# Kernel tuning notes

Measured on AMD Instinct MI355X. Metric: run time of the kernel, lower is better.

The kernel has to match this reference:

```python
import jax, jax.numpy as jnp
import numpy as np
import math

N = 8192
F_IN = 1024
F_OUT = 1024
MAX_ITER = 10


def whale_optimizer(positions, key, max_iter=MAX_ITER):
    """Vectorized whale optimization algorithm.

    Faithful to the original per-agent/per-dim update rules, but the agent
    loop is vectorized (on-device RNG, one parallel update per outer
    iteration); only the `max_iter` outer iterations stay sequential.
    positions: [N, D] float32.
    """
    n, d = positions.shape
    lower = jnp.min(positions)
    upper = jnp.max(positions)
    k0, loop_key = jax.random.split(key)
    leader = positions[jax.random.randint(k0, (), 0, n)]  # [D]

    def step(carry, it):
        pos, leader = carry
        itf = it.astype(jnp.float32)
        k = jax.random.fold_in(loop_key, it)
        k1, k2, k3, k4, k5, k6 = jax.random.split(k, 6)
        a = 2.0 - itf * (2.0 / max_iter)
        a2 = -1.0 + itf * (-1.0 / max_iter)
        r1 = jax.random.uniform(k1, (n, 1))
        r2 = jax.random.uniform(k2, (n, 1))
        A = 2.0 * a * r1 - a                       # [n,1]
        C = 2.0 * r2                               # [n,1]
        lp = (a2 - 1.0) * jax.random.uniform(k3, (n, 1)) + 1.0  # spiral param
        p = jax.random.uniform(k4, (n, 1))
        # random leader per (agent, dim), as in the original inner j-loop
        ridx = jax.random.randint(k5, (n, d), 0, n)
        x_rand = jnp.take_along_axis(pos, ridx, axis=0)         # [n,d]
        explore = jnp.abs(x_rand - A * jnp.abs(C * x_rand - pos))
        exploit = jnp.abs(leader - A * jnp.abs(C * leader - pos))
        spiral = jnp.abs(jnp.abs(leader - pos) * jnp.exp(lp) * jnp.cos(2.0 * jnp.pi * lp) + leader)
        new_pos = jnp.where(p < 0.5,
                            jnp.where(jnp.abs(A) >= 1.0, explore, exploit),
                            spiral)
        new_pos = jnp.clip(new_pos, lower, upper)
        new_leader = new_pos[jax.random.randint(k6, (), 0, n)]
        return (new_pos, new_leader), None

    (positions, _), _ = jax.lax.scan(step, (positions, leader), jnp.arange(max_iter))
    return positions


def setup_inputs() -> dict:
    key = jax.random.key(0)
    k1, k2, k3, k4 = jax.random.split(key, 4)
    stdv = 1.0 / math.sqrt(F_OUT)
    return {
        "input": jax.random.normal(k1, (N, F_IN), dtype=jnp.float32),
        "adj": jax.random.uniform(k2, (N, N), dtype=jnp.float32) * (1.0 / N),
        "h0": jax.random.normal(k3, (N, F_IN), dtype=jnp.float32),
        "weight": jax.random.uniform(k4, (F_IN, F_OUT), dtype=jnp.float32,
                                      minval=-stdv, maxval=stdv),
        "lamda": jnp.float32(0.5),
        "alpha": jnp.float32(0.1),
        "l": 1,
    }


def reference(input, adj, h0, weight, lamda, alpha, l):
    # variant=False, residual=False
    theta = jnp.log(lamda / l + 1.0)
    hi = adj @ input                                  # spmm(adj, input)
    support = (1.0 - alpha) * hi + alpha * h0
    r = support
    # original detaches support before the whale optimizer
    opt = whale_optimizer(jax.lax.stop_gradient(support), jax.random.key(42))
    output = theta * (opt @ weight) + (1.0 - theta) * r
    return output
```

## Files before the change

kernel.cpp:

```cpp
#include <hip/hip_runtime.h>
#include <hip/hip_bf16.h>
#include <stdint.h>
#include <math.h>

typedef uint32_t u32;
typedef __hip_bfloat16 bf16t;
typedef __attribute__((ext_vector_type(8))) short short8;
typedef __attribute__((ext_vector_type(4))) float f32x4;


__host__ __device__ __forceinline__ void tf2(u32 k0, u32 k1, u32 c0, u32 c1, u32& o0, u32& o1) {
  const u32 ks2 = k0 ^ k1 ^ 0x1BD11BDAu;
  u32 x0 = c0 + k0, x1 = c1 + k1;
#define TFROT(v,r) (((v)<<(r))|((v)>>(32-(r))))
#define TFR(r) { x0 += x1; x1 = TFROT(x1,r); x1 ^= x0; }
  TFR(13) TFR(15) TFR(26) TFR(6)   x0 += k1;  x1 += ks2 + 1u;
  TFR(17) TFR(29) TFR(16) TFR(24)  x0 += ks2; x1 += k0 + 2u;
  TFR(13) TFR(15) TFR(26) TFR(6)   x0 += k0;  x1 += k1 + 3u;
  TFR(17) TFR(29) TFR(16) TFR(24)  x0 += k1;  x1 += ks2 + 4u;
  TFR(13) TFR(15) TFR(26) TFR(6)   x0 += ks2; x1 += k0 + 5u;
#undef TFR
#undef TFROT
  o0 = x0; o1 = x1;
}

__host__ __device__ __forceinline__ float unif_row(u32 ka, u32 kb, int i) {
  u32 o0, o1;
  tf2(ka, kb, 0u, (u32)i, o0, o1);
  return __uint_as_float(0x3F800000u | ((o0 ^ o1) >> 9)) - 1.0f;
}

__device__ __forceinline__ int ridx_fn(u32 ka, u32 kb, u32 f) {
  u32 o0, o1; tf2(ka, kb, 0u, f, o0, o1); return (int)((o0 ^ o1) & 8191u);
}

static inline void split2(u32 ka, u32 kb, u32* kA, u32* kB) {
  u32 a0, a1, b0, b1;
  tf2(ka, kb, 0u, 0u, a0, a1);
  tf2(ka, kb, 0u, 1u, b0, b1);
  kA[0] = a0; kA[1] = a1; kB[0] = b0; kB[1] = b1;
}

static inline void split6(u32 ka, u32 kb, u32 out[6][2]) {
  for (u32 i = 0; i < 6; i++) { u32 o0, o1; tf2(ka, kb, 0u, i, o0, o1); out[i][0] = o0; out[i][1] = o1; }
}

static inline int scalar_randint8192(u32 ka, u32 kb) {
  u32 kA[2], kB[2];
  split2(ka, kb, kA, kB);
  u32 o0, o1;
  tf2(kB[0], kB[1], 0u, 0u, o0, o1);
  return (int)((o0 ^ o1) & 8191u);
}

__host__ __device__ __forceinline__ ushort f2bf(float f) {
  u32 u = __float_as_uint(f);
  u32 r = u + 0x7FFFu + ((u >> 16) & 1u);
  return (ushort)(r >> 16);
}

__device__ __forceinline__ void packa_body(int idx, const float* __restrict__ A, uint4* __restrict__ out,
                                           int K, int lgS) {
  const int S = K >> 6;
  const int chunk = idx >> 10;
  const int w = idx & 1023;
  const int r = w >> 3, kq = w & 7;
  const int cm = chunk >> lgS, s = chunk & (S - 1);
  const float* src = A + (size_t)((cm << 7) + r) * K + (s << 6) + (kq << 3);
  const float4 f0 = *(const float4*)src;
  const float4 f1 = *(const float4*)(src + 4);
  u32 wv[4];
  wv[0] = (u32)f2bf(f0.x) | ((u32)f2bf(f0.y) << 16);
  wv[1] = (u32)f2bf(f0.z) | ((u32)f2bf(f0.w) << 16);
  wv[2] = (u32)f2bf(f1.x) | ((u32)f2bf(f1.y) << 16);
  wv[3] = (u32)f2bf(f1.z) | ((u32)f2bf(f1.w) << 16);
  uint4 o; o.x = wv[0]; o.y = wv[1]; o.z = wv[2]; o.w = wv[3];
  out[((size_t)chunk << 10) + (r << 3) + (kq ^ (r & 7))] = o;
}

__device__ __forceinline__ void packb_body(int idx, const float* __restrict__ B, uint4* __restrict__ out,
                                           int Nn) {
  const int g = idx / Nn;
  const int n = idx - g * Nn;
  u32 wv[4];
#pragma unroll
  for (int j = 0; j < 4; j++) {
    const float f0 = B[(size_t)(g * 8 + 2 * j) * Nn + n];
    const float f1 = B[(size_t)(g * 8 + 2 * j + 1) * Nn + n];
    wv[j] = (u32)f2bf(f0) | ((u32)f2bf(f1) << 16);
  }
  uint4 o; o.x = wv[0]; o.y = wv[1]; o.z = wv[2]; o.w = wv[3];
  out[idx] = o;
}

__global__ __launch_bounds__(256) void pack_all_k(
    const float* __restrict__ adj, uint4* __restrict__ apk,
    const float* __restrict__ inp, uint4* __restrict__ b1p,
    const float* __restrict__ wgt, uint4* __restrict__ wp) {
  const int b = blockIdx.x;
  const int tid = threadIdx.x;
  if (b < 32768) {
    packa_body(b * 256 + tid, adj, apk, 8192, 7);
  } else if (b < 36864) {
    packb_body((b - 32768) * 256 + tid, inp, b1p, 1024);
  } else {
    packb_body((b - 36864) * 256 + tid, wgt, wp, 1024);
  }
}

__global__ __launch_bounds__(256) void minmax2_k(const float* __restrict__ part, int G, float* __restrict__ bnd) {
  __shared__ float slo[256], shi[256];
  const int tid = threadIdx.x;
  float lo = 3.4e38f, hi = -3.4e38f;
  for (int i = tid; i < G; i += 256) { lo = fminf(lo, part[i]); hi = fmaxf(hi, part[G + i]); }
  slo[tid] = lo; shi[tid] = hi; __syncthreads();
  for (int s = 128; s > 0; s >>= 1) {
    if (tid < s) { slo[tid] = fminf(slo[tid], slo[tid + s]); shi[tid] = fmaxf(shi[tid], shi[tid + s]); }
    __syncthreads();
  }
  if (tid == 0) { bnd[0] = slo[0]; bnd[1] = shi[0]; }
}

__device__ __forceinline__ void gld_lds16(const void* g, void* l) {
  __builtin_amdgcn_global_load_lds((const __attribute__((address_space(1))) void*)g,
                                   (__attribute__((address_space(3))) void*)l, 16, 0, 0);
}

template <int EPI>
__global__ __launch_bounds__(256, 2) void gemm_k(
    const bf16t* __restrict__ Ap, const bf16t* __restrict__ Bp,
    const float* __restrict__ aux, const float* __restrict__ sF,
    const int* __restrict__ sI, float* __restrict__ C,
    float* __restrict__ prt, int PG, int Nn, int K) {
  __shared__ __align__(16) bf16t As[2][8192];
  __shared__ __align__(16) bf16t Bs[2][8192];
  const int tid = threadIdx.x;
  const int lane = tid & 63;
  const int wave = tid >> 6;
  const int bm = blockIdx.x & 63;
  const int bn = blockIdx.x >> 6;
  const int m0 = bm << 7, n0 = bn << 7;
  const int wm = (wave & 1) << 6;
  const int wn = (wave >> 1) << 6;
  const int S = K >> 6;

  f32x4 acc[4][4];
#pragma unroll
  for (int i = 0; i < 4; i++)
#pragma unroll
    for (int j = 0; j < 4; j++) acc[i][j] = (f32x4){0.f, 0.f, 0.f, 0.f};

  const bf16t* gA0 = Ap + (((size_t)bm * S) << 13);
  const bf16t* gBj[4];
  const size_t bstep = (size_t)Nn * 64;
#pragma unroll
  for (int j = 0; j < 4; j++) {
    const int u = tid + (j << 8);
    gBj[j] = Bp + ((size_t)(u >> 7) * Nn + n0 + (u & 127)) * 8;
  }
  auto stage = [&](int s, int buf) {
    const bf16t* a = gA0 + ((size_t)s << 13);
#pragma unroll
    for (int j = 0; j < 4; j++) {
      const int u = tid + (j << 8);
      gld_lds16(a + ((size_t)u << 3), &As[buf][u << 3]);
    }
#pragma unroll
    for (int j = 0; j < 4; j++) {
      const int u = tid + (j << 8);
      gld_lds16(gBj[j] + (size_t)s * bstep, &Bs[buf][u << 3]);
    }
  };

  const int arow = lane & 15, aq = lane >> 4;
  const int abase = ((wm + arow) << 6) + ((aq ^ (arow & 7)) << 3);
  const int bbase = ((aq << 7) + wn + arow) << 3;

  stage(0, 0);

  for (int s = 0; s < S; ++s) {
    const int cur = s & 1;
    __syncthreads();
    if (s + 1 < S) stage(s + 1, cur ^ 1);
#pragma unroll
    for (int c = 0; c < 2; ++c) {
      short8 af[4], bv[4];
      const int ab = abase ^ (c << 5);
#pragma unroll
      for (int mt = 0; mt < 4; mt++)
        af[mt] = *(const short8*)(&As[cur][ab + mt * 1024]);
#pragma unroll
      for (int nt = 0; nt < 4; nt++)
        bv[nt] = *(const short8*)(&Bs[cur][bbase + (c << 12) + (nt << 7)]);
#pragma unroll
      for (int mt = 0; mt < 4; mt++)
#pragma unroll
        for (int nt = 0; nt < 4; nt++)
          acc[mt][nt] = __builtin_amdgcn_mfma_f32_16x16x32_bf16(af[mt], bv[nt], acc[mt][nt], 0, 0, 0);
    }
  }

  float p1, p2;
  if (EPI == 1) { const float al = sF[0]; p1 = 1.0f - al; p2 = al; }
  else { const float th = logf(sF[0] / (float)sI[0] + 1.0f); p1 = th; p2 = 1.0f - th; }
  const int col = lane & 15, rq = lane >> 4;
  float vlo = 3.4e38f, vhi = -3.4e38f;
#pragma unroll
  for (int mt = 0; mt < 4; mt++)
#pragma unroll
    for (int nt = 0; nt < 4; nt++)
#pragma unroll
      for (int r = 0; r < 4; r++) {
        const int gm = m0 + wm + mt * 16 + (rq << 2) + r;
        const int gn = n0 + wn + nt * 16 + col;
        const size_t ix = (size_t)gm * Nn + gn;
        const float v = p1 * acc[mt][nt][r] + p2 * aux[ix];
        C[ix] = v;
        if (EPI == 1) { vlo = fminf(vlo, v); vhi = fmaxf(vhi, v); }
      }
  if (EPI == 1) {
    __syncthreads();
    float* red = (float*)&As[0][0];
    red[tid] = vlo; red[256 + tid] = vhi;
    __syncthreads();
    for (int s = 128; s > 0; s >>= 1) {
      if (tid < s) {
        red[tid] = fminf(red[tid], red[tid + s]);
        red[256 + tid] = fmaxf(red[256 + tid], red[256 + tid + s]);
      }
      __syncthreads();
    }
    if (tid == 0) { prt[blockIdx.x] = red[0]; prt[PG + blockIdx.x] = red[256]; }
  }
}

struct WA {
  u32 k1a, k1b, k2a, k2b, k3a, k3b, k4a, k4b, k5a, k5b;
  int ldr;
  float a, a2;
};
struct WP { u32 k1a, k1b, k2a, k2b, k3a, k3b, k4a, k4b; float a, a2; int ldr; };
struct F5 { WP w[5]; };

__global__ __launch_bounds__(256) void whale_k(
    const float* __restrict__ pinb, float* __restrict__ poutb,
    ushort* __restrict__ opt, const float* __restrict__ bnd, WA w) {
  const int tid = threadIdx.x;
  const int wave = tid >> 6, lane = tid & 63;
  const int row = (blockIdx.x << 2) + wave;
  const float lo = bnd[0], hi = bnd[1];
  const float r1 = unif_row(w.k1a, w.k1b, row);
  const float r2 = unif_row(w.k2a, w.k2b, row);
  const float u3 = unif_row(w.k3a, w.k3b, row);
  const float p  = unif_row(w.k4a, w.k4b, row);
  float t2 = (2.0f * w.a) * r1;
  asm volatile("" : "+v"(t2));
  const float A = t2 - w.a;
  const float Cc = 2.0f * r2;
  const float* pin = pinb + ((size_t)row << 10);
  float4 pv[4];
#pragma unroll
  for (int k = 0; k < 4; ++k) pv[k] = *(const float4*)(pin + ((lane + (k << 6)) << 2));

  float ov[4][4];
  const bool bp = (p < 0.5f);
  const bool ex = bp && (fabsf(A) >= 1.0f);
  if (ex) {
    int ri[4][4];
#pragma unroll
    for (int k = 0; k < 4; ++k) {
      const u32 fb = ((u32)row << 10) + (u32)((lane + (k << 6)) << 2);
#pragma unroll
      for (int e = 0; e < 4; ++e) ri[k][e] = ridx_fn(w.k5a, w.k5b, fb + (u32)e);
    }
    float xr[4][4];
#pragma unroll
    for (int k = 0; k < 4; ++k) {
      const int j0 = (lane + (k << 6)) << 2;
#pragma unroll
      for (int e = 0; e < 4; ++e) xr[k][e] = pinb[((size_t)ri[k][e] << 10) + j0 + e];
    }
#pragma unroll
    for (int k = 0; k < 4; ++k)
#pragma unroll
      for (int e = 0; e < 4; ++e) {
        const float pos = (&pv[k].x)[e];
        ov[k][e] = fabsf(xr[k][e] - A * fabsf(Cc * xr[k][e] - pos));
      }
  } else {
    const float* ldp = pinb + ((size_t)w.ldr << 10);
    float4 lv[4];
#pragma unroll
    for (int k = 0; k < 4; ++k) lv[k] = *(const float4*)(ldp + ((lane + (k << 6)) << 2));
    if (bp) {
#pragma unroll
      for (int k = 0; k < 4; ++k)
#pragma unroll
        for (int e = 0; e < 4; ++e) {
          const float pos = (&pv[k].x)[e], ld = (&lv[k].x)[e];
          ov[k][e] = fabsf(ld - A * fabsf(Cc * ld - pos));
        }
    } else {
      const float lp = (w.a2 - 1.0f) * u3 + 1.0f;
      const float s1 = expf(lp);
      const float s2 = cosf(6.2831855f * lp);
#pragma unroll
      for (int k = 0; k < 4; ++k)
#pragma unroll
        for (int e = 0; e < 4; ++e) {
          const float pos = (&pv[k].x)[e], ld = (&lv[k].x)[e];
          ov[k][e] = fabsf(fabsf(ld - pos) * s1 * s2 + ld);
        }
    }
  }
#pragma unroll
  for (int k = 0; k < 4; ++k) {
    const int j0 = (lane + (k << 6)) << 2;
    float4 res;
#pragma unroll
    for (int e = 0; e < 4; ++e) (&res.x)[e] = fminf(fmaxf(ov[k][e], lo), hi);
    if (!opt) {
      *(float4*)(poutb + ((size_t)row << 10) + j0) = res;
    } else {
      ushort4 o4;
      o4.x = f2bf(res.x); o4.y = f2bf(res.y); o4.z = f2bf(res.z); o4.w = f2bf(res.w);
      const int rw = row & 127;
      const size_t chunk = (size_t)((row >> 7) << 4) + (j0 >> 6);
      ushort* dst = opt + (chunk << 13) + (rw << 6) + ((((j0 >> 3) & 7) ^ (rw & 7)) << 3) + (j0 & 7);
      *(ushort4*)dst = o4;
    }
  }
}

template <int NK>
__device__ __forceinline__ void upd_row(const WP w, int row, float lo, float hi,
                                        const float4* lv, float4* x) {
  const float r1 = unif_row(w.k1a, w.k1b, row);
  const float r2 = unif_row(w.k2a, w.k2b, row);
  const float u3 = unif_row(w.k3a, w.k3b, row);
  const float p  = unif_row(w.k4a, w.k4b, row);
  float t2 = (2.0f * w.a) * r1;
  asm volatile("" : "+v"(t2));
  const float A = t2 - w.a;
  const float Cc = 2.0f * r2;
  const bool bp = (p < 0.5f);
  float s1 = 0.f, s2 = 0.f;
  if (!bp) {
    const float lp = (w.a2 - 1.0f) * u3 + 1.0f;
    s1 = expf(lp);
    s2 = cosf(6.2831855f * lp);
  }
#pragma unroll
  for (int k = 0; k < NK; ++k)
#pragma unroll
    for (int e = 0; e < 4; ++e) {
      const float pos = (&x[k].x)[e], ld = (&lv[k].x)[e];
      const float ov = bp ? fabsf(ld - A * fabsf(Cc * ld - pos))
                          : fabsf(fabsf(ld - pos) * s1 * s2 + ld);
      (&x[k].x)[e] = fminf(fmaxf(ov, lo), hi);
    }
}

__global__ __launch_bounds__(256) void ldrchain_k(
    const float* __restrict__ p4, const float* __restrict__ bnd,
    float* __restrict__ V, F5 f) {
  const int j0 = threadIdx.x << 2;
  const float lo = bnd[0], hi = bnd[1];
  float4 v[5];
  v[0] = *(const float4*)(p4 + ((size_t)f.w[0].ldr << 10) + j0);
  *(float4*)(V + j0) = v[0];
#pragma unroll
  for (int t = 1; t < 5; ++t) {
    const int row = f.w[t].ldr;
    float4 x = *(const float4*)(p4 + ((size_t)row << 10) + j0);
#pragma unroll
    for (int q = 0; q < t; ++q) upd_row<1>(f.w[q], row, lo, hi, &v[q], &x);
    v[t] = x;
    *(float4*)(V + (t << 10) + j0) = x;
  }
}

__global__ __launch_bounds__(256) void fused5_k(
    const float* __restrict__ p4, const float* __restrict__ V,
    const float* __restrict__ bnd, ushort* __restrict__ opt, F5 f) {
  const int tid = threadIdx.x;
  const int wave = tid >> 6, lane = tid & 63;
  const int row = (blockIdx.x << 2) + wave;
  const float lo = bnd[0], hi = bnd[1];
  const float* pin = p4 + ((size_t)row << 10);
  float4 x[4];
#pragma unroll
  for (int k = 0; k < 4; ++k) x[k] = *(const float4*)(pin + ((lane + (k << 6)) << 2));
#pragma unroll
  for (int it = 0; it < 5; ++it) {
    float4 lv[4];
#pragma unroll
    for (int k = 0; k < 4; ++k)
      lv[k] = *(const float4*)(V + (it << 10) + ((lane + (k << 6)) << 2));
    upd_row<4>(f.w[it], row, lo, hi, lv, x);
  }
#pragma unroll
  for (int k = 0; k < 4; ++k) {
    const int j0 = (lane + (k << 6)) << 2;
    ushort4 o4;
    o4.x = f2bf(x[k].x); o4.y = f2bf(x[k].y); o4.z = f2bf(x[k].z); o4.w = f2bf(x[k].w);
    const int rw = row & 127;
    const size_t chunk = (size_t)((row >> 7) << 4) + (j0 >> 6);
    ushort* dst = opt + (chunk << 13) + (rw << 6) + ((((j0 >> 3) & 7) ^ (rw & 7)) << 3) + (j0 & 7);
    *(ushort4*)dst = o4;
  }
}

extern "C" void kernel_launch(void* const* d_in, const int* in_sizes, int n_in,
                              void* d_out, int out_size, void* d_ws, size_t ws_size,
                              hipStream_t stream) {
  const float* inp = (const float*)d_in[0];
  const float* adj = (const float*)d_in[1];
  const float* h0  = (const float*)d_in[2];
  const float* wgt = (const float*)d_in[3];
  const float* lam = (const float*)d_in[4];
  const float* alp = (const float*)d_in[5];
  const int* lint  = (const int*)d_in[6];

  float* outp = (float*)d_out;

  char* ws = (char*)d_ws;
  bf16t* Apk  = (bf16t*)(ws);
  float* P0   = (float*)(ws);
  float* P1   = (float*)(ws + 33554432);
  ushort* OPT = (ushort*)(ws + 67108864);
  bf16t* B1p  = (bf16t*)(ws + 134217728);
  bf16t* Wp   = (bf16t*)(ws + 150994944);
  float* SUP  = (float*)(ws + 153092096);
  float* PRT  = (float*)(ws + 186646528);
  float* BND  = (float*)(ws + 186662912);
  float* LDRV = (float*)(ws + 186663168);

  hipLaunchKernelGGL(pack_all_k, dim3(37376), dim3(256), 0, stream,
                     adj, (uint4*)Apk, inp, (uint4*)B1p, wgt, (uint4*)Wp);
  hipLaunchKernelGGL((gemm_k<1>), dim3(512), dim3(256), 0, stream, Apk, B1p, h0, alp, lint,
                     SUP, PRT, 512, 1024, 8192);
  hipLaunchKernelGGL(minmax2_k, dim3(1), dim3(256), 0, stream, PRT, 512, BND);

  u32 k0k[2], lpk[2];
  split2(0u, 42u, k0k, lpk);
  int ldr = scalar_randint8192(k0k[0], k0k[1]);
  WA wa[10];
  for (int it = 0; it < 10; ++it) {
    u32 ka, kb; tf2(lpk[0], lpk[1], 0u, (u32)it, ka, kb);
    u32 ks[6][2];
    split6(ka, kb, ks);
    u32 k5A[2], k5B[2];
    split2(ks[4][0], ks[4][1], k5A, k5B);
    WA& w = wa[it];
    w.k1a = ks[0][0]; w.k1b = ks[0][1];
    w.k2a = ks[1][0]; w.k2b = ks[1][1];
    w.k3a = ks[2][0]; w.k3b = ks[2][1];
    w.k4a = ks[3][0]; w.k4b = ks[3][1];
    w.k5a = k5B[0];   w.k5b = k5B[1];
    w.ldr = ldr;
    const float itf = (float)it;
    w.a = 2.0f - itf * 0.2f;
    w.a2 = -1.0f + itf * (-0.1f);
    ldr = scalar_randint8192(ks[5][0], ks[5][1]);
  }
  bool safe5 = true;
  for (int r = 0; r < 8192 && safe5; ++r) {
    u32 o0, o1; tf2(wa[5].k1a, wa[5].k1b, 0u, (u32)r, o0, o1);
    if (((o0 ^ o1) >> 9) == 0u) safe5 = false;
  }

  const float* cur = SUP;
  float* bufs[2] = {P0, P1};
  for (int it = 0; it < 5; ++it) {
    float* nxt = bufs[it & 1];
    hipLaunchKernelGGL(whale_k, dim3(2048), dim3(256), 0, stream, cur, nxt,
                       (ushort*)nullptr, BND, wa[it]);
    cur = nxt;
  }
  if (safe5) {
    F5 f;
    for (int t = 0; t < 5; ++t) {
      const WA& w = wa[5 + t];
      f.w[t].k1a = w.k1a; f.w[t].k1b = w.k1b;
      f.w[t].k2a = w.k2a; f.w[t].k2b = w.k2b;
      f.w[t].k3a = w.k3a; f.w[t].k3b = w.k3b;
      f.w[t].k4a = w.k4a; f.w[t].k4b = w.k4b;
      f.w[t].a = w.a; f.w[t].a2 = w.a2; f.w[t].ldr = w.ldr;
    }
    hipLaunchKernelGGL(ldrchain_k, dim3(1), dim3(256), 0, stream, cur, BND, LDRV, f);
    hipLaunchKernelGGL(fused5_k, dim3(2048), dim3(256), 0, stream, cur, LDRV, BND, OPT, f);
  } else {
    for (int it = 5; it < 10; ++it) {
      float* nxt = bufs[it & 1];
      hipLaunchKernelGGL(whale_k, dim3(2048), dim3(256), 0, stream, cur, nxt,
                         (it == 9) ? OPT : (ushort*)nullptr, BND, wa[it]);
      cur = nxt;
    }
  }
  hipLaunchKernelGGL((gemm_k<2>), dim3(512), dim3(256), 0, stream, (const bf16t*)OPT, Wp, SUP, lam, lint,
                     outp, (float*)nullptr, 0, 1024, 1024);
  (void)in_sizes; (void)n_in; (void)out_size; (void)ws_size;
}
```

Baseline: 857.0 us.

## Fuse fp32-to-bf16 conversion of adj into the first GEMM's A-tile loading

Removes the separate pack pass that converted the 8192x8192 fp32 adjacency matrix to a swizzled bf16 layout. The first GEMM now loads fp32 A tiles straight from global memory into registers and converts them with v_cvt_pk_bf16_f32. The next tile's loads are issued before the MFMA loop and written to LDS after it, so load latency overlaps compute. This drops a 256MB read plus a 128MB write and re-read of packed data, but raises register pressure and puts the conversion and LDS stores inside the GEMM main loop.

```diff
diff --git a/kernel.cpp b/kernel.cpp
--- a/kernel.cpp
+++ b/kernel.cpp
@@ -59,25 +59,6 @@
   return (ushort)(r >> 16);
 }
 
-__device__ __forceinline__ void packa_body(int idx, const float* __restrict__ A, uint4* __restrict__ out,
-                                           int K, int lgS) {
-  const int S = K >> 6;
-  const int chunk = idx >> 10;
-  const int w = idx & 1023;
-  const int r = w >> 3, kq = w & 7;
-  const int cm = chunk >> lgS, s = chunk & (S - 1);
-  const float* src = A + (size_t)((cm << 7) + r) * K + (s << 6) + (kq << 3);
-  const float4 f0 = *(const float4*)src;
-  const float4 f1 = *(const float4*)(src + 4);
-  u32 wv[4];
-  wv[0] = (u32)f2bf(f0.x) | ((u32)f2bf(f0.y) << 16);
-  wv[1] = (u32)f2bf(f0.z) | ((u32)f2bf(f0.w) << 16);
-  wv[2] = (u32)f2bf(f1.x) | ((u32)f2bf(f1.y) << 16);
-  wv[3] = (u32)f2bf(f1.z) | ((u32)f2bf(f1.w) << 16);
-  uint4 o; o.x = wv[0]; o.y = wv[1]; o.z = wv[2]; o.w = wv[3];
-  out[((size_t)chunk << 10) + (r << 3) + (kq ^ (r & 7))] = o;
-}
-
 __device__ __forceinline__ void packb_body(int idx, const float* __restrict__ B, uint4* __restrict__ out,
                                            int Nn) {
   const int g = idx / Nn;
@@ -94,17 +75,14 @@
 }
 
 __global__ __launch_bounds__(256) void pack_all_k(
-    const float* __restrict__ adj, uint4* __restrict__ apk,
     const float* __restrict__ inp, uint4* __restrict__ b1p,
     const float* __restrict__ wgt, uint4* __restrict__ wp) {
   const int b = blockIdx.x;
   const int tid = threadIdx.x;
-  if (b < 32768) {
-    packa_body(b * 256 + tid, adj, apk, 8192, 7);
-  } else if (b < 36864) {
-    packb_body((b - 32768) * 256 + tid, inp, b1p, 1024);
+  if (b < 4096) {
+    packb_body(b * 256 + tid, inp, b1p, 1024);
   } else {
-    packb_body((b - 36864) * 256 + tid, wgt, wp, 1024);
+    packb_body((b - 4096) * 256 + tid, wgt, wp, 1024);
   }
 }
 
@@ -126,9 +104,15 @@
                                    (__attribute__((address_space(3))) void*)l, 16, 0, 0);
 }
 
-template <int EPI>
+__device__ __forceinline__ u32 cvtpk2(float lo, float hi) {
+  u32 r;
+  asm("v_cvt_pk_bf16_f32 %0, %1, %2" : "=v"(r) : "v"(lo), "v"(hi));
+  return r;
+}
+
+template <int EPI, int AF32>
 __global__ __launch_bounds__(256, 2) void gemm_k(
-    const bf16t* __restrict__ Ap, const bf16t* __restrict__ Bp,
+    const void* __restrict__ Araw, const bf16t* __restrict__ Bp,
     const float* __restrict__ aux, const float* __restrict__ sF,
     const int* __restrict__ sI, float* __restrict__ C,
     float* __restrict__ prt, int PG, int Nn, int K) {
@@ -150,7 +134,9 @@
 #pragma unroll
     for (int j = 0; j < 4; j++) acc[i][j] = (f32x4){0.f, 0.f, 0.f, 0.f};
 
-  const bf16t* gA0 = Ap + (((size_t)bm * S) << 13);
+  const float* Af = (const float*)Araw;
+  const bf16t* Ab = (const bf16t*)Araw;
+
   const bf16t* gBj[4];
   const size_t bstep = (size_t)Nn * 64;
 #pragma unroll
@@ -158,17 +144,43 @@
     const int u = tid + (j << 8);
     gBj[j] = Bp + ((size_t)(u >> 7) * Nn + n0 + (u & 127)) * 8;
   }
-  auto stage = [&](int s, int buf) {
+  auto stageB = [&](int s, int buf) {
+#pragma unroll
+    for (int j = 0; j < 4; j++) {
+      const int u = tid + (j << 8);
+      gld_lds16(gBj[j] + (size_t)s * bstep, &Bs[buf][u << 3]);
+    }
+  };
+  const bf16t* gA0 = Ab + (((size_t)bm * S) << 13);
+  auto stageA0 = [&](int s, int buf) {
     const bf16t* a = gA0 + ((size_t)s << 13);
 #pragma unroll
     for (int j = 0; j < 4; j++) {
       const int u = tid + (j << 8);
       gld_lds16(a + ((size_t)u << 3), &As[buf][u << 3]);
     }
+  };
+  const int ar = tid >> 1;
+  const int ac = (tid & 1) << 5;
+  float4 a32[8];
+  auto issueA1 = [&](int s) {
+    const float* p = Af + (size_t)(m0 + ar) * K + (s << 6) + ac;
 #pragma unroll
     for (int j = 0; j < 4; j++) {
-      const int u = tid + (j << 8);
-      gld_lds16(gBj[j] + (size_t)s * bstep, &Bs[buf][u << 3]);
+      a32[2 * j]     = *(const float4*)(p + j * 8);
+      a32[2 * j + 1] = *(const float4*)(p + j * 8 + 4);
+    }
+  };
+  auto writeA1 = [&](int buf) {
+#pragma unroll
+    for (int j = 0; j < 4; j++) {
+      uint4 o;
+      o.x = cvtpk2(a32[2 * j].x,     a32[2 * j].y);
+      o.y = cvtpk2(a32[2 * j].z,     a32[2 * j].w);
+      o.z = cvtpk2(a32[2 * j + 1].x, a32[2 * j + 1].y);
+      o.w = cvtpk2(a32[2 * j + 1].z, a32[2 * j + 1].w);
+      const int kq = ((tid & 1) << 2) + j;
+      *(uint4*)(&As[buf][((ar << 3) + (kq ^ (ar & 7))) << 3]) = o;
     }
   };
 
@@ -176,12 +188,17 @@
   const int abase = ((wm + arow) << 6) + ((aq ^ (arow & 7)) << 3);
   const int bbase = ((aq << 7) + wn + arow) << 3;
 
-  stage(0, 0);
+  if (AF32) { issueA1(0); stageB(0, 0); writeA1(0); }
+  else      { stageA0(0, 0); stageB(0, 0); }
 
   for (int s = 0; s < S; ++s) {
     const int cur = s & 1;
     __syncthreads();
-    if (s + 1 < S) stage(s + 1, cur ^ 1);
+    const bool more = (s + 1 < S);
+    if (more) {
+      if (AF32) { issueA1(s + 1); stageB(s + 1, cur ^ 1); }
+      else      { stageA0(s + 1, cur ^ 1); stageB(s + 1, cur ^ 1); }
+    }
 #pragma unroll
     for (int c = 0; c < 2; ++c) {
       short8 af[4], bv[4];
@@ -198,6 +215,7 @@
         for (int nt = 0; nt < 4; nt++)
           acc[mt][nt] = __builtin_amdgcn_mfma_f32_16x16x32_bf16(af[mt], bv[nt], acc[mt][nt], 0, 0, 0);
     }
+    if (more && AF32) writeA1(cur ^ 1);
   }
 
   float p1, p2;
@@ -425,7 +443,6 @@
   float* outp = (float*)d_out;
 
   char* ws = (char*)d_ws;
-  bf16t* Apk  = (bf16t*)(ws);
   float* P0   = (float*)(ws);
   float* P1   = (float*)(ws + 33554432);
   ushort* OPT = (ushort*)(ws + 67108864);
@@ -436,9 +453,9 @@
   float* BND  = (float*)(ws + 186662912);
   float* LDRV = (float*)(ws + 186663168);
 
-  hipLaunchKernelGGL(pack_all_k, dim3(37376), dim3(256), 0, stream,
-                     adj, (uint4*)Apk, inp, (uint4*)B1p, wgt, (uint4*)Wp);
-  hipLaunchKernelGGL((gemm_k<1>), dim3(512), dim3(256), 0, stream, Apk, B1p, h0, alp, lint,
+  hipLaunchKernelGGL(pack_all_k, dim3(4608), dim3(256), 0, stream,
+                     inp, (uint4*)B1p, wgt, (uint4*)Wp);
+  hipLaunchKernelGGL((gemm_k<1, 1>), dim3(512), dim3(256), 0, stream, (const void*)adj, B1p, h0, alp, lint,
                      SUP, PRT, 512, 1024, 8192);
   hipLaunchKernelGGL(minmax2_k, dim3(1), dim3(256), 0, stream, PRT, 512, BND);
 
@@ -498,7 +515,7 @@
       cur = nxt;
     }
   }
-  hipLaunchKernelGGL((gemm_k<2>), dim3(512), dim3(256), 0, stream, (const bf16t*)OPT, Wp, SUP, lam, lint,
+  hipLaunchKernelGGL((gemm_k<2, 0>), dim3(512), dim3(256), 0, stream, (const void*)OPT, Wp, SUP, lam, lint,
                      outp, (float*)nullptr, 0, 1024, 1024);
   (void)in_sizes; (void)n_in; (void)out_size; (void)ws_size;
 }
```

New measurement: 1.006 ms. 1.17x slower.
